# Optimization experiments

Measured on AMD Instinct MI355X. Metric: run time of the kernel, lower is better.

Reference implementation:

```python
import jax, jax.numpy as jnp
import numpy as np

WS = 7        # window size
IMG = 56      # input resolution (H = W)
BATCH = 32    # image batch
DIM = 384
HEADS = 12
HEAD_DIM = DIM // HEADS
N = WS * WS                      # tokens per window = 49
NW = (IMG // WS) * (IMG // WS)   # windows per image = 64
B_ = BATCH * NW                  # 2048
TBL = (2 * WS - 1) ** 2          # 169


def _rel_index(ws):
    # standard Swin relative position index, values in [0, (2ws-1)^2)
    coords = np.stack(np.meshgrid(np.arange(ws), np.arange(ws), indexing='ij'))
    coords = coords.reshape(2, -1)                       # (2, N)
    rel = coords[:, :, None] - coords[:, None, :]        # (2, N, N)
    rel = rel.transpose(1, 2, 0).astype(np.int64).copy()
    rel[:, :, 0] += ws - 1
    rel[:, :, 1] += ws - 1
    rel[:, :, 0] *= 2 * ws - 1
    return rel.sum(-1)                                   # (N, N)


def _shift_mask(H, W, ws, shift):
    # shifted-window attention mask, (nW, N, N) with 0 / -100
    img = np.zeros((H, W))
    cnt = 0
    for hs in (slice(0, -ws), slice(-ws, -shift), slice(-shift, None)):
        for wsl in (slice(0, -ws), slice(-ws, -shift), slice(-shift, None)):
            img[hs, wsl] = cnt
            cnt += 1
    win = img.reshape(H // ws, ws, W // ws, ws).transpose(0, 2, 1, 3).reshape(-1, ws * ws)
    diff = win[:, None, :] - win[:, :, None]
    return np.where(diff != 0, -100.0, 0.0).astype(np.float32)


def setup_inputs() -> dict:
    key = jax.random.key(0)
    ks = jax.random.split(key, 7)
    s = 0.02
    return {
        'x': jax.random.normal(ks[0], (B_, N, DIM), jnp.float32),
        'mask': jnp.asarray(_shift_mask(IMG, IMG, WS, WS // 2)),
        'rpe_indices': jnp.asarray(_rel_index(WS)),
        'qkv_w': jax.random.normal(ks[1], (3 * DIM, DIM), jnp.float32) * s,
        'qkv_b': jnp.zeros((3 * DIM,), jnp.float32),
        'proj_w': jax.random.normal(ks[2], (DIM, DIM), jnp.float32) * s,
        'proj_b': jnp.zeros((DIM,), jnp.float32),
        'q_rpe': jax.random.normal(ks[3], (HEADS, HEAD_DIM, TBL), jnp.float32) * s,
        'k_rpe': jax.random.normal(ks[4], (HEADS, HEAD_DIM, TBL), jnp.float32) * s,
        'v_rpe': jax.random.normal(ks[5], (HEADS, TBL, HEAD_DIM), jnp.float32) * s,
    }


def reference(x, mask, rpe_indices, qkv_w, qkv_b, proj_w, proj_b, q_rpe, k_rpe, v_rpe):
    B, n, C = x.shape
    h, hd = q_rpe.shape[0], q_rpe.shape[1]
    scale = hd ** -0.5

    qkv = x @ qkv_w.T + qkv_b                                   # (B, N, 3C)
    qkv = qkv.reshape(B, n, 3, h, hd).transpose(2, 0, 3, 1, 4)   # (3, B, h, N, hd)
    q, k, v = qkv[0] * scale, qkv[1], qkv[2]

    attn = jnp.einsum('bhid,bhjd->bhij', q, k)                   # (B, h, N, N)

    # Contextual q/k bias. The torch code does b_q.flatten(2)[:, :, rpe_indices]
    # with rpe_indices in [0, TBL): gathering from the flattened (N*TBL) axis with
    # indices < TBL selects row 0 of the N axis, i.e. b_q[:, :, 0, rpe_indices].
    # We compute only that row, which is mathematically identical.
    bq0 = jnp.einsum('bhd,hdt->bht', q[:, :, 0], q_rpe)          # (B, h, TBL)
    bk0 = jnp.einsum('bhd,hdt->bht', k[:, :, 0], k_rpe)          # (B, h, TBL)
    attn = attn + (bq0 + bk0)[:, :, rpe_indices]                 # gather -> (B, h, N, N)

    nW = mask.shape[0]
    attn = attn.reshape(B // nW, nW, h, n, n) + mask[None, :, None]
    attn = jax.nn.softmax(attn.reshape(B, h, n, n), axis=-1)

    # contextual v bias: w = v_rpe[:, rpe_indices] -> (h, N, N, hd)
    w = v_rpe[:, rpe_indices.reshape(-1)].reshape(h, n, n, hd)
    r_v = jnp.einsum('bhij,hijd->bihd', attn, w).reshape(B, n, C)

    out = jnp.einsum('bhij,bhjd->bihd', attn, v).reshape(B, n, C) + r_v
    out = out @ proj_w.T + proj_b
    return out, attn
```

## Files before the change

### kernel.cpp

```cpp
#include <hip/hip_runtime.h>


typedef unsigned int u32;
typedef unsigned short u16;
typedef __attribute__((ext_vector_type(8))) short bf16x8;
typedef __attribute__((ext_vector_type(4))) float f32x4;
typedef float f4a __attribute__((ext_vector_type(4), aligned(4)));

#define SCALE 0.17677669529663687f

__device__ __forceinline__ u16 f2b(float f) {
  union { float f; u32 u; } c; c.f = f;
  u32 u = c.u;
  return (u16)((u + 0x7FFFu + ((u >> 16) & 1u)) >> 16);
}
__device__ __forceinline__ float b2f(u16 s) {
  union { float f; u32 u; } c; c.u = ((u32)s) << 16;
  return c.f;
}
__device__ __forceinline__ void async16(void* lds, const void* g) {
  __builtin_amdgcn_global_load_lds(
      (const __attribute__((address_space(1))) u32*)g,
      (__attribute__((address_space(3))) u32*)lds, 16, 0, 0);
}

__global__ __launch_bounds__(256) void k_cast(const float* __restrict__ s,
                                              u16* __restrict__ d, int n4) {
  int i = blockIdx.x * 256 + threadIdx.x;
  int str = gridDim.x * 256;
  for (; i < n4; i += str) {
    float4 v = ((const float4*)s)[i];
    ushort4 o;
    o.x = f2b(v.x); o.y = f2b(v.y); o.z = f2b(v.z); o.w = f2b(v.w);
    ((ushort4*)d)[i] = o;
  }
}

__global__ __launch_bounds__(256) void k_mbi(const float* __restrict__ mask,
                                             const int* __restrict__ idx,
                                             u16* __restrict__ mbi) {
  int i = blockIdx.x * 256 + threadIdx.x;
  if (i >= 64 * 2401) return;
  int p = i % 2401;
  mbi[i] = (u16)(idx[p] | ((mask[i] != 0.0f) ? 256 : 0));
}

__global__ __launch_bounds__(256) void k_qkv(
    const u16* __restrict__ A, const u16* __restrict__ Bw,
    const float* __restrict__ bias, u16* __restrict__ outq) {
  int bx = blockIdx.x;
  int mt = bx / 9, nt = bx - mt * 9;
  size_t m0 = (size_t)mt * 128;
  int n0 = nt * 128;
  int tid = threadIdx.x;
  int w = tid >> 6, l = tid & 63;
  int wm = w >> 1, wn = w & 1;
  int lr = l & 15, lg = l >> 4, lk8 = lg << 3;
  __shared__ u16 At[128 * 32];
  __shared__ u16 Bt[128 * 32];
  f32x4 acc[4][4] = {};
  int row = tid >> 2, c8 = (tid & 3) << 3;
  const u16* gA = A + (m0 + row) * 384 + c8;
  const u16* gA2 = A + (m0 + row + 64) * 384 + c8;
  const u16* gB = Bw + (size_t)(n0 + row) * 384 + c8;
  const u16* gB2 = Bw + (size_t)(n0 + row + 64) * 384 + c8;
  for (int ks = 0; ks < 12; ++ks) {
    int k0 = ks * 32;
    async16(At + tid * 8, gA + k0);
    async16(At + (256 + tid) * 8, gA2 + k0);
    async16(Bt + tid * 8, gB + k0);
    async16(Bt + (256 + tid) * 8, gB2 + k0);
    __syncthreads();
    bf16x8 af[4], bfr[4];
#pragma unroll
    for (int mi = 0; mi < 4; ++mi)
      af[mi] = *(const bf16x8*)&At[(wm * 64 + mi * 16 + lr) * 32 + lk8];
#pragma unroll
    for (int ni = 0; ni < 4; ++ni)
      bfr[ni] = *(const bf16x8*)&Bt[(wn * 64 + ni * 16 + lr) * 32 + lk8];
#pragma unroll
    for (int mi = 0; mi < 4; ++mi)
#pragma unroll
      for (int ni = 0; ni < 4; ++ni)
        acc[mi][ni] = __builtin_amdgcn_mfma_f32_16x16x32_bf16(af[mi], bfr[ni], acc[mi][ni], 0, 0, 0);
    __syncthreads();
  }
#pragma unroll
  for (int ni = 0; ni < 4; ++ni) {
    int cc = n0 + wn * 64 + ni * 16 + lr;
    float bv = bias[cc];
    float sc = (cc < 384) ? SCALE : 1.0f;
#pragma unroll
    for (int mi = 0; mi < 4; ++mi)
#pragma unroll
      for (int r = 0; r < 4; ++r) {
        size_t rr = m0 + wm * 64 + mi * 16 + lg * 4 + r;
        outq[rr * 1152 + cc] = f2b((acc[mi][ni][r] + bv) * sc);
      }
  }
}

__global__ __launch_bounds__(256) void k_bqk(
    const u16* __restrict__ qkv, const float* __restrict__ q_rpe,
    const float* __restrict__ k_rpe, float* __restrict__ bqk) {
  int bx = blockIdx.x;
  int mtile = bx / 12, h = bx % 12;
  int b0 = mtile * 64;
  int tid = threadIdx.x;
  int w = tid >> 6, l = tid & 63;
  int lr = l & 15, g = l >> 4;

  __shared__ __align__(16) u16 At[64 * 64];
  __shared__ __align__(16) u16 Bt[192 * 64];

  {
    int m = tid >> 2;
#pragma unroll
    for (int rnd = 0; rnd < 2; ++rnd) {
      int c = (tid & 3) + rnd * 4;
      const u16* src = qkv + (size_t)(b0 + m) * 56448 + h * 32 +
                       ((c < 4) ? c * 8 : 384 + (c - 4) * 8);
      bf16x8 v = *(const bf16x8*)src;
      int byte = (m * 128 + c * 16) ^ ((m & 7) << 4);
      *(bf16x8*)((char*)At + byte) = v;
    }
  }
  if (tid < 192) {
    int t = tid;
#pragma unroll
    for (int c = 0; c < 8; ++c) {
      u16 pk[8];
#pragma unroll
      for (int e = 0; e < 8; ++e) {
        int d = (c & 3) * 8 + e;
        float v = 0.f;
        if (t < 169)
          v = (c < 4) ? q_rpe[(h * 32 + d) * 169 + t]
                      : k_rpe[(h * 32 + d) * 169 + t];
        pk[e] = f2b(v);
      }
      int byte = (t * 128 + c * 16) ^ ((t & 7) << 4);
      *(bf16x8*)((char*)Bt + byte) = *(bf16x8*)pk;
    }
  }
  __syncthreads();

  f32x4 acc[12] = {};
  bf16x8 af[2];
#pragma unroll
  for (int ks = 0; ks < 2; ++ks) {
    int row = w * 16 + lr;
    af[ks] = *(const bf16x8*)((const char*)At +
              ((row * 128 + ks * 64 + g * 16) ^ ((row & 7) << 4)));
  }
#pragma unroll
  for (int nt = 0; nt < 12; ++nt) {
#pragma unroll
    for (int ks = 0; ks < 2; ++ks) {
      int t = nt * 16 + lr;
      bf16x8 bf = *(const bf16x8*)((const char*)Bt +
                   ((t * 128 + ks * 64 + g * 16) ^ ((t & 7) << 4)));
      acc[nt] = __builtin_amdgcn_mfma_f32_16x16x32_bf16(af[ks], bf, acc[nt], 0, 0, 0);
    }
  }
#pragma unroll
  for (int nt = 0; nt < 12; ++nt) {
    int t = nt * 16 + lr;
    if (t < 169) {
#pragma unroll
      for (int r = 0; r < 4; ++r) {
        int b = b0 + w * 16 + g * 4 + r;
        bqk[((size_t)b * 12 + h) * 169 + t] = acc[nt][r];
      }
    }
  }
}

__global__ __launch_bounds__(256) void k_attn(
    const u16* __restrict__ qkv, const float* __restrict__ bqkG,
    const u16* __restrict__ mbi,
    float* __restrict__ attn, u16* __restrict__ o1) {
  int blk = blockIdx.x;
  int b = blk / 3, hg = blk % 3;
  int tid = threadIdx.x, w = tid >> 6, l = tid & 63;
  int h = hg * 4 + w;
  int lr = l & 15, g = l >> 4;

  __shared__ __align__(16) char R[32704];
  __shared__ __align__(16) u16 vL[4][2048];
  u16* mbiL = (u16*)R;
  float* bqkL = (float*)(R + 4832);
  u16* pL = (u16*)(R + 7600);
  float* aS = (float*)R;

  const u16* qbase = qkv + (size_t)b * 49 * 1152 + h * 32;
  const u16* kbase = qbase + 384;
  const u16* vbase = qbase + 768;

  {
    const u16* mrow = mbi + (size_t)(b & 63) * 2401;
    for (int p = tid; p < 2401; p += 256) mbiL[p] = mrow[p];
  }
  u16* vw = &vL[w][0];
#pragma unroll
  for (int p = 0; p < 4; ++p) {
    int j = p * 16 + (l >> 2);
    int jr = (j < 49) ? j : 48;
    async16(vw + p * 512 + l * 8, vbase + (size_t)jr * 1152 + (l & 3) * 8);
  }
  {
    const float* bg = bqkG + ((size_t)b * 12 + h) * 169;
#pragma unroll
    for (int t0 = 0; t0 < 192; t0 += 64) {
      int t = t0 + l;
      if (t < 169) bqkL[w * 172 + t] = bg[t];
    }
  }

  bf16x8 qf[4], kf[4];
#pragma unroll
  for (int t = 0; t < 4; ++t) {
    int qi = t * 16 + lr;
    int qir = (qi < 49) ? qi : 48;
    qf[t] = *(const bf16x8*)(qbase + (size_t)qir * 1152 + g * 8);
    kf[t] = *(const bf16x8*)(kbase + (size_t)qir * 1152 + g * 8);
  }

  f32x4 S[4][4] = {};
#pragma unroll
  for (int mt = 0; mt < 4; ++mt)
#pragma unroll
    for (int nt = 0; nt < 4; ++nt)
      S[mt][nt] = __builtin_amdgcn_mfma_f32_16x16x32_bf16(kf[mt], qf[nt], S[mt][nt], 0, 0, 0);

  __syncthreads();

#pragma unroll
  for (int nt = 0; nt < 4; ++nt) {
    int qi = nt * 16 + lr;
#pragma unroll
    for (int mt = 0; mt < 4; ++mt)
#pragma unroll
      for (int r = 0; r < 4; ++r) {
        int kj = mt * 16 + g * 4 + r;
        float s = S[mt][nt][r];
        if (qi < 49 && kj < 49) {
          u16 t = mbiL[qi * 49 + kj];
          s += bqkL[w * 172 + (t & 255)] - 100.f * (float)(t >> 8);
        } else {
          s = -1e9f;
        }
        S[mt][nt][r] = s;
      }
  }

  float rinv[4];
#pragma unroll
  for (int nt = 0; nt < 4; ++nt) {
    float m = -1e30f;
#pragma unroll
    for (int mt = 0; mt < 4; ++mt)
#pragma unroll
      for (int r = 0; r < 4; ++r) m = fmaxf(m, S[mt][nt][r]);
    m = fmaxf(m, __shfl_xor(m, 16, 64));
    m = fmaxf(m, __shfl_xor(m, 32, 64));
    float sum = 0.f;
#pragma unroll
    for (int mt = 0; mt < 4; ++mt)
#pragma unroll
      for (int r = 0; r < 4; ++r) {
        float e = __expf(S[mt][nt][r] - m);
        S[mt][nt][r] = e;
        sum += e;
      }
    sum += __shfl_xor(sum, 16, 64);
    sum += __shfl_xor(sum, 32, 64);
    rinv[nt] = 1.f / sum;
  }

  u16* pw = pL + w * 3136;
#pragma unroll
  for (int nt = 0; nt < 4; ++nt) {
    int qi = nt * 16 + lr;
    if (qi < 49) {
      int swz = (qi & 7) << 4;
#pragma unroll
      for (int mt = 0; mt < 4; ++mt) {
        u32 w0 = (u32)f2b(S[mt][nt][0]) | ((u32)f2b(S[mt][nt][1]) << 16);
        u32 w1 = (u32)f2b(S[mt][nt][2]) | ((u32)f2b(S[mt][nt][3]) << 16);
        int off = (qi * 128 + mt * 32 + g * 8) ^ swz;
        uint2 pk = {w0, w1};
        *(uint2*)((char*)pw + off) = pk;
      }
    }
  }

  f32x4 O[2][4] = {};
#pragma unroll
  for (int ks = 0; ks < 2; ++ks) {
    bf16x8 pb[4];
#pragma unroll
    for (int nti = 0; nti < 4; ++nti) {
      int qi = nti * 16 + lr;
      int qir = (qi < 49) ? qi : 48;
      int off = (qir * 128 + ks * 64 + g * 16) ^ ((qir & 7) << 4);
      pb[nti] = *(const bf16x8*)((const char*)pw + off);
    }
    bf16x8 va[2];
#pragma unroll
    for (int mtd = 0; mtd < 2; ++mtd)
#pragma unroll
      for (int jj = 0; jj < 8; ++jj)
        va[mtd][jj] = (short)vw[(ks * 32 + g * 8 + jj) * 32 + mtd * 16 + lr];
#pragma unroll
    for (int mtd = 0; mtd < 2; ++mtd)
#pragma unroll
      for (int nti = 0; nti < 4; ++nti)
        O[mtd][nti] = __builtin_amdgcn_mfma_f32_16x16x32_bf16(va[mtd], pb[nti], O[mtd][nti], 0, 0, 0);
  }

  {
    u16* ob = o1 + (size_t)b * 49 * 384 + h * 32;
#pragma unroll
    for (int nti = 0; nti < 4; ++nti) {
      int i = nti * 16 + lr;
      if (i < 49) {
        float riv = rinv[nti];
#pragma unroll
        for (int mtd = 0; mtd < 2; ++mtd) {
          u32 w0 = (u32)f2b(O[mtd][nti][0] * riv) | ((u32)f2b(O[mtd][nti][1] * riv) << 16);
          u32 w1 = (u32)f2b(O[mtd][nti][2] * riv) | ((u32)f2b(O[mtd][nti][3] * riv) << 16);
          uint2 pk = {w0, w1};
          *(uint2*)&ob[(size_t)i * 384 + mtd * 16 + g * 4] = pk;
        }
      }
    }
  }

  __syncthreads();
  float* aw = aS + w * 1216;
  float* ao = attn + (size_t)(b * 12 + h) * 2401;
#pragma unroll
  for (int half = 0; half < 2; ++half) {
    int lo = half * 1204;
#pragma unroll
    for (int nt = 0; nt < 4; ++nt) {
      int qi = nt * 16 + lr;
      if (qi < 49) {
        float riv = rinv[nt];
#pragma unroll
        for (int mt = 0; mt < 4; ++mt)
#pragma unroll
          for (int r = 0; r < 4; ++r) {
            int kj = mt * 16 + g * 4 + r;
            if (kj < 49) {
              int p = qi * 49 + kj - lo;
              if (p >= 0 && p < 1204) aw[p] = S[mt][nt][r] * riv;
            }
          }
      }
    }
    asm volatile("s_waitcnt lgkmcnt(0)" ::: "memory");
    int lim = half ? 1197 : 1204;
#pragma unroll
    for (int it = 0; it < 19; ++it) {
      int p = l + it * 64;
      if (p < lim) ao[lo + p] = aw[p];
    }
    asm volatile("s_waitcnt lgkmcnt(0)" ::: "memory");
  }
}

__global__ __launch_bounds__(256) void k_rv(
    const float* __restrict__ attn, const int* __restrict__ idx,
    const float* __restrict__ v_rpe, u16* __restrict__ o1) {
  int bx = blockIdx.x;
  int bc = bx & 7;
  int hi = bx >> 3;
  int i = hi % 49, h = hi / 49;
  int b0 = bc * 256;
  int tid = threadIdx.x;
  int w = tid >> 6, l = tid & 63;
  int lr = l & 15, g = l >> 4;

  __shared__ __align__(16) u16 aB[256 * 64];
  __shared__ __align__(16) u16 wT[32 * 64];

  if (tid < 196) {
    int j = tid >> 2, d0 = (tid & 3) * 8;
    const float* vr = v_rpe + ((size_t)h * 169 + idx[i * 49 + j]) * 32 + d0;
    float4 a = *(const float4*)vr;
    float4 bvv = *(const float4*)(vr + 4);
    float el[8] = {a.x, a.y, a.z, a.w, bvv.x, bvv.y, bvv.z, bvv.w};
#pragma unroll
    for (int e = 0; e < 8; ++e) {
      int d = d0 + e;
      int byte = (d * 128 + j * 2) ^ ((d & 7) << 4);
      *(u16*)((char*)wT + byte) = f2b(el[e]);
    }
  } else {
    int t = tid - 196;
    int j = 49 + (t >> 2), d0 = (t & 3) * 8;
#pragma unroll
    for (int e = 0; e < 8; ++e) {
      int d = d0 + e;
      int byte = (d * 128 + j * 2) ^ ((d & 7) << 4);
      *(u16*)((char*)wT + byte) = 0;
    }
  }

  {
    int bl = tid;
    const float* ar = attn + ((size_t)(b0 + bl) * 12 + h) * 2401 + (size_t)i * 49;
    f4a fv[12];
#pragma unroll
    for (int q = 0; q < 12; ++q) fv[q] = *(const f4a*)(ar + q * 4);
    float tail = ar[48];
    u32 wd[32];
#pragma unroll
    for (int k = 0; k < 24; ++k)
      wd[k] = (u32)f2b(fv[k >> 1][(k & 1) * 2]) |
              ((u32)f2b(fv[k >> 1][(k & 1) * 2 + 1]) << 16);
    wd[24] = (u32)f2b(tail);
#pragma unroll
    for (int k = 25; k < 32; ++k) wd[k] = 0;
#pragma unroll
    for (int q = 0; q < 8; ++q) {
      int byte = (bl * 128 + q * 16) ^ ((bl & 7) << 4);
      *(uint4*)((char*)aB + byte) = *(uint4*)&wd[q * 4];
    }
  }
  __syncthreads();

  f32x4 acc[2][4] = {};
#pragma unroll
  for (int ks = 0; ks < 2; ++ks) {
    bf16x8 af[2], bfr[4];
#pragma unroll
    for (int mt = 0; mt < 2; ++mt) {
      int d = mt * 16 + lr;
      int byte = (d * 128 + ks * 64 + g * 16) ^ ((d & 7) << 4);
      af[mt] = *(const bf16x8*)((const char*)wT + byte);
    }
#pragma unroll
    for (int nt = 0; nt < 4; ++nt) {
      int row = w * 64 + nt * 16 + lr;
      int byte = (row * 128 + ks * 64 + g * 16) ^ ((row & 7) << 4);
      bfr[nt] = *(const bf16x8*)((const char*)aB + byte);
    }
#pragma unroll
    for (int mt = 0; mt < 2; ++mt)
#pragma unroll
      for (int nt = 0; nt < 4; ++nt)
        acc[mt][nt] = __builtin_amdgcn_mfma_f32_16x16x32_bf16(af[mt], bfr[nt], acc[mt][nt], 0, 0, 0);
  }

#pragma unroll
  for (int nt = 0; nt < 4; ++nt) {
    int bl = w * 64 + nt * 16 + lr;
    u16* ob = o1 + ((size_t)(b0 + bl) * 49 + i) * 384 + h * 32;
#pragma unroll
    for (int mt = 0; mt < 2; ++mt) {
      int d = mt * 16 + g * 4;
      uint2 old = *(uint2*)&ob[d];
      uint2 nw;
      nw.x = (u32)f2b(b2f((u16)(old.x & 0xffff)) + acc[mt][nt][0]) |
             ((u32)f2b(b2f((u16)(old.x >> 16)) + acc[mt][nt][1]) << 16);
      nw.y = (u32)f2b(b2f((u16)(old.y & 0xffff)) + acc[mt][nt][2]) |
             ((u32)f2b(b2f((u16)(old.y >> 16)) + acc[mt][nt][3]) << 16);
      *(uint2*)&ob[d] = nw;
    }
  }
}

__global__ __launch_bounds__(256) void k_proj(
    const u16* __restrict__ A, const u16* __restrict__ Bw,
    const float* __restrict__ bias, float* __restrict__ out) {
  int bx = blockIdx.x;
  int mt = bx / 3, nt = bx - mt * 3;
  size_t m0 = (size_t)mt * 128;
  int n0 = nt * 128;
  int tid = threadIdx.x;
  int w = tid >> 6, l = tid & 63;
  int wm = w >> 1, wn = w & 1;
  int lr = l & 15, lg = l >> 4, lk8 = lg << 3;
  __shared__ u16 At[128 * 32];
  __shared__ u16 Bt[128 * 32];
  f32x4 acc[4][4] = {};
  int row = tid >> 2, c8 = (tid & 3) << 3;
  const u16* gA = A + (m0 + row) * 384 + c8;
  const u16* gA2 = A + (m0 + row + 64) * 384 + c8;
  const u16* gB = Bw + (size_t)(n0 + row) * 384 + c8;
  const u16* gB2 = Bw + (size_t)(n0 + row + 64) * 384 + c8;
  for (int ks = 0; ks < 12; ++ks) {
    int k0 = ks * 32;
    async16(At + tid * 8, gA + k0);
    async16(At + (256 + tid) * 8, gA2 + k0);
    async16(Bt + tid * 8, gB + k0);
    async16(Bt + (256 + tid) * 8, gB2 + k0);
    __syncthreads();
    bf16x8 af[4], bfr[4];
#pragma unroll
    for (int mi = 0; mi < 4; ++mi)
      af[mi] = *(const bf16x8*)&At[(wm * 64 + mi * 16 + lr) * 32 + lk8];
#pragma unroll
    for (int ni = 0; ni < 4; ++ni)
      bfr[ni] = *(const bf16x8*)&Bt[(wn * 64 + ni * 16 + lr) * 32 + lk8];
#pragma unroll
    for (int mi = 0; mi < 4; ++mi)
#pragma unroll
      for (int ni = 0; ni < 4; ++ni)
        acc[mi][ni] = __builtin_amdgcn_mfma_f32_16x16x32_bf16(af[mi], bfr[ni], acc[mi][ni], 0, 0, 0);
    __syncthreads();
  }
#pragma unroll
  for (int mi = 0; mi < 4; ++mi)
#pragma unroll
    for (int ni = 0; ni < 4; ++ni)
#pragma unroll
      for (int r = 0; r < 4; ++r) {
        int rr = wm * 64 + mi * 16 + lg * 4 + r;
        int cc = wn * 64 + ni * 16 + lr;
        out[(m0 + rr) * 384 + (size_t)(n0 + cc)] = acc[mi][ni][r] + bias[n0 + cc];
      }
}

extern "C" void kernel_launch(void* const* d_in, const int* in_sizes, int n_in,
                              void* d_out, int out_size, void* d_ws, size_t ws_size,
                              hipStream_t stream) {
  const float* x      = (const float*)d_in[0];
  const float* mask   = (const float*)d_in[1];
  const int*   rpe    = (const int*)d_in[2];
  const float* qkv_w  = (const float*)d_in[3];
  const float* qkv_b  = (const float*)d_in[4];
  const float* proj_w = (const float*)d_in[5];
  const float* proj_b = (const float*)d_in[6];
  const float* q_rpe  = (const float*)d_in[7];
  const float* k_rpe  = (const float*)d_in[8];
  const float* v_rpe  = (const float*)d_in[9];

  float* out  = (float*)d_out;
  float* attn = out + (size_t)100352 * 384;
  float* bqkG = out;

  char* ws = (char*)d_ws;
  u16* qkvb   = (u16*)ws;
  u16* wqkvb  = (u16*)(ws + 231211008);
  u16* wprojb = (u16*)(ws + 232095744);
  u16* mbi    = (u16*)(ws + 232390656);
  u16* xb     = (u16*)(ws + 232697984);
  u16* o1     = xb;

  k_cast<<<2048, 256, 0, stream>>>(x, xb, 9633792);
  k_cast<<<432, 256, 0, stream>>>(qkv_w, wqkvb, 110592);
  k_cast<<<144, 256, 0, stream>>>(proj_w, wprojb, 36864);
  k_mbi<<<601, 256, 0, stream>>>(mask, rpe, mbi);
  k_qkv<<<7056, 256, 0, stream>>>(xb, wqkvb, qkv_b, qkvb);
  k_bqk<<<384, 256, 0, stream>>>(qkvb, q_rpe, k_rpe, bqkG);
  k_attn<<<6144, 256, 0, stream>>>(qkvb, bqkG, mbi, attn, o1);
  k_rv<<<4704, 256, 0, stream>>>(attn, rpe, v_rpe, o1);
  k_proj<<<2352, 256, 0, stream>>>(o1, wprojb, proj_b, out);
}
```

Baseline: 589.2 us.

## Stage bf16 padded attention copy for rv pass and swizzle block order

The attention kernel now also writes a padded (49x64) bf16 copy of the normalized probabilities into the output buffer region, which is later overwritten by projection. k_rv reads its MFMA B-operand fragments directly from that compact bf16 buffer instead of re-reading fp32 attention rows and staging them through LDS. This halves the bytes k_rv reads and removes its LDS staging. The cost is an extra global write in k_attn. Separately, k_qkv, k_attn and k_proj remap block indices across 8 groups, likely to spread work over XCDs and improve cache locality. bqkG moves into the workspace to avoid clobbering.

```diff
diff --git a/kernel.cpp b/kernel.cpp
--- a/kernel.cpp
+++ b/kernel.cpp
@@ -5,7 +5,6 @@
 typedef unsigned short u16;
 typedef __attribute__((ext_vector_type(8))) short bf16x8;
 typedef __attribute__((ext_vector_type(4))) float f32x4;
-typedef float f4a __attribute__((ext_vector_type(4), aligned(4)));
 
 #define SCALE 0.17677669529663687f
 
@@ -48,7 +47,8 @@
 __global__ __launch_bounds__(256) void k_qkv(
     const u16* __restrict__ A, const u16* __restrict__ Bw,
     const float* __restrict__ bias, u16* __restrict__ outq) {
-  int bx = blockIdx.x;
+  int bx0 = blockIdx.x;
+  int bx = (bx0 & 7) * 882 + (bx0 >> 3);
   int mt = bx / 9, nt = bx - mt * 9;
   size_t m0 = (size_t)mt * 128;
   int n0 = nt * 128;
@@ -179,8 +179,9 @@
 __global__ __launch_bounds__(256) void k_attn(
     const u16* __restrict__ qkv, const float* __restrict__ bqkG,
     const u16* __restrict__ mbi,
-    float* __restrict__ attn, u16* __restrict__ o1) {
-  int blk = blockIdx.x;
+    float* __restrict__ attn, u16* __restrict__ attnB, u16* __restrict__ o1) {
+  int blk0 = blockIdx.x;
+  int blk = (blk0 & 7) * 768 + (blk0 >> 3);
   int b = blk / 3, hg = blk % 3;
   int tid = threadIdx.x, w = tid >> 6, l = tid & 63;
   int h = hg * 4 + w;
@@ -278,6 +279,24 @@
     rinv[nt] = 1.f / sum;
   }
 
+  {
+    u16* abase = attnB + ((size_t)(b * 12 + h) * 49) * 64;
+#pragma unroll
+    for (int nt = 0; nt < 4; ++nt) {
+      int qi = nt * 16 + lr;
+      if (qi < 49) {
+        float riv = rinv[nt];
+#pragma unroll
+        for (int mt = 0; mt < 4; ++mt) {
+          u32 w0 = (u32)f2b(S[mt][nt][0] * riv) | ((u32)f2b(S[mt][nt][1] * riv) << 16);
+          u32 w1 = (u32)f2b(S[mt][nt][2] * riv) | ((u32)f2b(S[mt][nt][3] * riv) << 16);
+          uint2 pk = {w0, w1};
+          *(uint2*)(abase + (size_t)qi * 64 + mt * 16 + g * 4) = pk;
+        }
+      }
+    }
+  }
+
   u16* pw = pL + w * 3136;
 #pragma unroll
   for (int nt = 0; nt < 4; ++nt) {
@@ -372,7 +391,7 @@
 }
 
 __global__ __launch_bounds__(256) void k_rv(
-    const float* __restrict__ attn, const int* __restrict__ idx,
+    const u16* __restrict__ attnB, const int* __restrict__ idx,
     const float* __restrict__ v_rpe, u16* __restrict__ o1) {
   int bx = blockIdx.x;
   int bc = bx & 7;
@@ -383,7 +402,6 @@
   int w = tid >> 6, l = tid & 63;
   int lr = l & 15, g = l >> 4;
 
-  __shared__ __align__(16) u16 aB[256 * 64];
   __shared__ __align__(16) u16 wT[32 * 64];
 
   if (tid < 196) {
@@ -408,28 +426,6 @@
       *(u16*)((char*)wT + byte) = 0;
     }
   }
-
-  {
-    int bl = tid;
-    const float* ar = attn + ((size_t)(b0 + bl) * 12 + h) * 2401 + (size_t)i * 49;
-    f4a fv[12];
-#pragma unroll
-    for (int q = 0; q < 12; ++q) fv[q] = *(const f4a*)(ar + q * 4);
-    float tail = ar[48];
-    u32 wd[32];
-#pragma unroll
-    for (int k = 0; k < 24; ++k)
-      wd[k] = (u32)f2b(fv[k >> 1][(k & 1) * 2]) |
-              ((u32)f2b(fv[k >> 1][(k & 1) * 2 + 1]) << 16);
-    wd[24] = (u32)f2b(tail);
-#pragma unroll
-    for (int k = 25; k < 32; ++k) wd[k] = 0;
-#pragma unroll
-    for (int q = 0; q < 8; ++q) {
-      int byte = (bl * 128 + q * 16) ^ ((bl & 7) << 4);
-      *(uint4*)((char*)aB + byte) = *(uint4*)&wd[q * 4];
-    }
-  }
   __syncthreads();
 
   f32x4 acc[2][4] = {};
@@ -445,8 +441,8 @@
 #pragma unroll
     for (int nt = 0; nt < 4; ++nt) {
       int row = w * 64 + nt * 16 + lr;
-      int byte = (row * 128 + ks * 64 + g * 16) ^ ((row & 7) << 4);
-      bfr[nt] = *(const bf16x8*)((const char*)aB + byte);
+      const u16* ar = attnB + (((size_t)(b0 + row) * 12 + h) * 49 + i) * 64;
+      bfr[nt] = *(const bf16x8*)(ar + ks * 32 + g * 8);
     }
 #pragma unroll
     for (int mt = 0; mt < 2; ++mt)
@@ -476,7 +472,8 @@
 __global__ __launch_bounds__(256) void k_proj(
     const u16* __restrict__ A, const u16* __restrict__ Bw,
     const float* __restrict__ bias, float* __restrict__ out) {
-  int bx = blockIdx.x;
+  int bx0 = blockIdx.x;
+  int bx = (bx0 & 7) * 294 + (bx0 >> 3);
   int mt = bx / 3, nt = bx - mt * 3;
   size_t m0 = (size_t)mt * 128;
   int n0 = nt * 128;
@@ -539,17 +536,18 @@
   const float* k_rpe  = (const float*)d_in[8];
   const float* v_rpe  = (const float*)d_in[9];
 
-  float* out  = (float*)d_out;
-  float* attn = out + (size_t)100352 * 384;
-  float* bqkG = out;
+  float* out   = (float*)d_out;
+  float* attn  = out + (size_t)100352 * 384;
+  u16*   attnB = (u16*)d_out;
 
   char* ws = (char*)d_ws;
-  u16* qkvb   = (u16*)ws;
-  u16* wqkvb  = (u16*)(ws + 231211008);
-  u16* wprojb = (u16*)(ws + 232095744);
-  u16* mbi    = (u16*)(ws + 232390656);
-  u16* xb     = (u16*)(ws + 232697984);
-  u16* o1     = xb;
+  u16*   qkvb   = (u16*)ws;
+  u16*   wqkvb  = (u16*)(ws + 231211008);
+  u16*   wprojb = (u16*)(ws + 232095744);
+  u16*   mbi    = (u16*)(ws + 232390656);
+  float* bqkG   = (float*)(ws + 232697984);
+  u16*   xb     = (u16*)(ws + 249311360);
+  u16*   o1     = xb;
 
   k_cast<<<2048, 256, 0, stream>>>(x, xb, 9633792);
   k_cast<<<432, 256, 0, stream>>>(qkv_w, wqkvb, 110592);
@@ -557,7 +555,7 @@
   k_mbi<<<601, 256, 0, stream>>>(mask, rpe, mbi);
   k_qkv<<<7056, 256, 0, stream>>>(xb, wqkvb, qkv_b, qkvb);
   k_bqk<<<384, 256, 0, stream>>>(qkvb, q_rpe, k_rpe, bqkG);
-  k_attn<<<6144, 256, 0, stream>>>(qkvb, bqkG, mbi, attn, o1);
-  k_rv<<<4704, 256, 0, stream>>>(attn, rpe, v_rpe, o1);
+  k_attn<<<6144, 256, 0, stream>>>(qkvb, bqkG, mbi, attn, attnB, o1);
+  k_rv<<<4704, 256, 0, stream>>>(attnB, rpe, v_rpe, o1);
   k_proj<<<2352, 256, 0, stream>>>(o1, wprojb, proj_b, out);
 }
```

New measurement: 602.2 us. 2.2% more time.
